# Optimization experiments

Measured on AMD Instinct MI355X. Metric: run time of the kernel, lower is better.

Reference implementation:

```python
import jax, jax.numpy as jnp
import numpy as np

B, D, H, W, C = 2, 8, 56, 56, 384
NH = 12
HD = C // NH
WIN = (2, 7, 7)
SHIFT = (1, 3, 3)
TDIM = 384
RANK = C // 8
HID = 4 * C
N = WIN[0] * WIN[1] * WIN[2]  # 98 tokens per window
NW = (D // WIN[0]) * (H // WIN[1]) * (W // WIN[2])  # windows per batch element


def _rel_index():
    wd, wh, ww = WIN
    coords = np.stack(np.meshgrid(np.arange(wd), np.arange(wh), np.arange(ww), indexing='ij'))
    coords = coords.reshape(3, -1)  # (3, N)
    rel = (coords[:, :, None] - coords[:, None, :]).transpose(1, 2, 0)  # (N, N, 3)
    rel[..., 0] += wd - 1; rel[..., 1] += wh - 1; rel[..., 2] += ww - 1
    rel[..., 0] *= (2 * wh - 1) * (2 * ww - 1)
    rel[..., 1] *= (2 * ww - 1)
    return rel.sum(-1)  # (N, N) int

REL_IDX = _rel_index()


def _wpart_np(x):
    b, d, h, w, c = x.shape
    x = x.reshape(b, d // WIN[0], WIN[0], h // WIN[1], WIN[1], w // WIN[2], WIN[2], c)
    return x.transpose(0, 1, 3, 5, 2, 4, 6, 7).reshape(-1, N, c)


def _attn_mask():
    # faithful port of compute_mask (note: only 2 slices along W, as in source)
    wd, wh, ww = WIN
    sd, sh, sw = SHIFT
    img = np.zeros((1, D, H, W, 1), np.float32)
    cnt = 0
    for ds in (slice(-wd), slice(-wd, -sd), slice(-sd, None)):
        for hs in (slice(-wh), slice(-wh, -sh), slice(-sh, None)):
            for ws in (slice(-ww), slice(-ww, None)):
                img[:, ds, hs, ws, :] = cnt
                cnt += 1
    mw = _wpart_np(img).squeeze(-1)  # (nW, N)
    am = mw[:, None, :] - mw[:, :, None]  # (nW, N, N)
    return np.where(am != 0, np.float32(-100.0), np.float32(0.0))

ATTN_MASK = _attn_mask()


def wpart(x):
    b, c = x.shape[0], x.shape[-1]
    x = x.reshape(b, D // WIN[0], WIN[0], H // WIN[1], WIN[1], W // WIN[2], WIN[2], c)
    return x.transpose(0, 1, 3, 5, 2, 4, 6, 7).reshape(-1, N, c)


def wrev(win):
    c = win.shape[-1]
    x = win.reshape(B, D // WIN[0], H // WIN[1], W // WIN[2], WIN[0], WIN[1], WIN[2], c)
    return x.transpose(0, 1, 4, 2, 5, 3, 6, 7).reshape(B, D, H, W, c)


def ln(x):
    m = x.mean(-1, keepdims=True)
    v = ((x - m) ** 2).mean(-1, keepdims=True)
    return (x - m) / jnp.sqrt(v + 1e-6)


def window_attn(xw, qkv_w, qkv_b, proj_w, proj_b, rel_bias, mask):
    Bw = xw.shape[0]
    qkv = (xw @ qkv_w + qkv_b).reshape(Bw, N, 3, NH, HD).transpose(2, 0, 3, 1, 4)
    q, k, v = qkv[0] * (HD ** -0.5), qkv[1], qkv[2]
    a = jnp.einsum('bhnd,bhmd->bhnm', q, k)  # (Bw, NH, N, N)
    bias = rel_bias[REL_IDX.reshape(-1)].reshape(N, N, NH).transpose(2, 0, 1)
    a = a + bias[None]
    a = a.reshape(Bw // NW, NW, NH, N, N) + mask[None, :, None]
    a = jax.nn.softmax(a.reshape(Bw, NH, N, N), axis=-1)
    out = jnp.einsum('bhnm,bhmd->bhnd', a, v).transpose(0, 2, 1, 3).reshape(Bw, N, C)
    return out @ proj_w + proj_b


def setup_inputs() -> dict:
    key = jax.random.key(0)
    ks = jax.random.split(key, 16)
    s = 0.02
    return {
        'x': jax.random.normal(ks[0], (B, D, H, W, C), jnp.float32),
        't': jax.random.normal(ks[1], (B, TDIM), jnp.float32),
        'qkv_w': jax.random.normal(ks[2], (C, 3 * C), jnp.float32) * s,
        'qkv_b': jax.random.normal(ks[3], (3 * C,), jnp.float32) * s,
        'proj_w': jax.random.normal(ks[4], (C, C), jnp.float32) * s,
        'proj_b': jax.random.normal(ks[5], (C,), jnp.float32) * s,
        'rel_bias': jax.random.normal(ks[6], ((2 * WIN[0] - 1) * (2 * WIN[1] - 1) * (2 * WIN[2] - 1), NH), jnp.float32) * s,
        'fc1_w': jax.random.normal(ks[7], (C, HID), jnp.float32) * s,
        'fc1_b': jax.random.normal(ks[8], (HID,), jnp.float32) * s,
        'fc2_w': jax.random.normal(ks[9], (HID, C), jnp.float32) * s,
        'fc2_b': jax.random.normal(ks[10], (C,), jnp.float32) * s,
        'ada_w1': jax.random.normal(ks[11], (TDIM, RANK), jnp.float32) * s,
        'ada_w2': jax.random.normal(ks[12], (RANK, 6 * C), jnp.float32) * s,
        'ada_b2': jax.random.normal(ks[13], (6 * C,), jnp.float32) * s,
    }


def reference(x, t, qkv_w, qkv_b, proj_w, proj_b, rel_bias, fc1_w, fc1_b, fc2_w, fc2_b, ada_w1, ada_w2, ada_b2):
    mask = jnp.asarray(ATTN_MASK)
    mod = jax.nn.silu(t) @ ada_w1 @ ada_w2 + ada_b2  # (B, 6C)
    s_msa, sc_msa, g_msa, s_mlp, sc_mlp, g_mlp = jnp.split(mod, 6, axis=1)

    def mod5(h, sh, sc):
        return h * (1 + sc[:, None, None, None, :]) + sh[:, None, None, None, :]

    # attention branch (shifted-window MSA)
    h = mod5(ln(x), s_msa, sc_msa)
    hs = jnp.roll(h, shift=(-SHIFT[0], -SHIFT[1], -SHIFT[2]), axis=(1, 2, 3))
    aw = window_attn(wpart(hs), qkv_w, qkv_b, proj_w, proj_b, rel_bias, mask)
    hs = wrev(aw)
    h = jnp.roll(hs, shift=SHIFT, axis=(1, 2, 3))
    x = x + g_msa[:, None, None, None, :] * h

    # MLP branch
    h2 = mod5(ln(x), s_mlp, sc_mlp)
    m = jax.nn.gelu(h2 @ fc1_w + fc1_b, approximate=False) @ fc2_w + fc2_b
    return x + g_mlp[:, None, None, None, :] * m
```

## Files before the change

### kernel.cpp

```cpp
#include <hip/hip_runtime.h>
#include <hip/hip_bf16.h>
#include <math.h>

using bf16 = __hip_bfloat16;
typedef __bf16 bf16x8 __attribute__((ext_vector_type(8)));
typedef float f32x4 __attribute__((ext_vector_type(4)));
typedef unsigned int u32;


__device__ __forceinline__ void async_cp16(const void* g, void* l) {
  __builtin_amdgcn_global_load_lds(
      (const __attribute__((address_space(1))) u32*)g,
      (__attribute__((address_space(3))) u32*)l, 16, 0, 0);
}

__device__ __forceinline__ int row_to_gidx(int row) {
  int win = row / 98, tok = row - win * 98;
  int b = win >> 8, wd = (win >> 6) & 3, wh = (win >> 3) & 7, ww = win & 7;
  int td = tok / 49, rem = tok - td * 49;
  int th = rem / 7, tw = rem - th * 7;
  int od = (wd * 2 + td + 1) & 7;
  int oh = wh * 7 + th + 3; if (oh >= 56) oh -= 56;
  int ow = ww * 7 + tw + 3; if (ow >= 56) ow -= 56;
  return ((b * 8 + od) * 56 + oh) * 56 + ow;
}

__global__ __launch_bounds__(256) void mod_kernel(
    const float* __restrict__ t, const float* __restrict__ w1,
    const float* __restrict__ w2, const float* __restrict__ b2,
    float* __restrict__ modout)
{
  __shared__ float u[2 * 48];
  int tid = threadIdx.x;
  if (tid < 96) {
    int b = tid / 48, r = tid - (tid / 48) * 48;
    float acc = 0.f;
    for (int k = 0; k < 384; ++k) {
      float x = t[b * 384 + k];
      float s = x / (1.f + __expf(-x));
      acc += s * w1[k * 48 + r];
    }
    u[b * 48 + r] = acc;
  }
  __syncthreads();
  for (int idx = tid; idx < 2 * 2304; idx += 256) {
    int b = idx / 2304, c = idx - b * 2304;
    float acc = b2[c];
    #pragma unroll
    for (int k = 0; k < 48; ++k) acc += u[b * 48 + k] * w2[k * 2304 + c];
    modout[idx] = acc;
  }
}

__global__ __launch_bounds__(256) void wconv_frag_kernel(
    const float* __restrict__ W, bf16* __restrict__ Wf, int K, int N)
{
  int idx = blockIdx.x * 256 + threadIdx.x;
  if (idx >= K * N) return;
  int k = idx / N, n = idx - (idx / N) * N;
  int ntile = n >> 4, kstep = k >> 5;
  int l = (n & 15) + (((k >> 3) & 3) << 4);
  size_t dst = (((size_t)(ntile * (K >> 5) + kstep)) << 9) + (l << 3) + (k & 7);
  Wf[dst] = __float2bfloat16(W[idx]);
}

__global__ __launch_bounds__(256) void bm_kernel(
    const float* __restrict__ relb, bf16* __restrict__ bm)
{
  int idx = blockIdx.x * 256 + threadIdx.x;
  if (idx >= 4 * 12 * 112 * 112) return;
  int j = idx % 112, tmp = idx / 112;
  int i = tmp % 112; tmp /= 112;
  int h = tmp % 12, p = tmp / 12;
  float v;
  if (i < 98 && j < 98) {
    int tdi = i / 49, ri = i % 49, thi = ri / 7, twi = ri % 7;
    int tdj = j / 49, rj = j % 49, thj = rj / 7, twj = rj % 7;
    int ridx = (tdi - tdj + 1) * 169 + (thi - thj + 6) * 13 + (twi - twj + 6);
    bool msk = ((p & 2) && (tdi != tdj)) || ((p & 1) && ((thi < 4) != (thj < 4)));
    v = relb[ridx * 12 + h] + (msk ? -100.f : 0.f);
  } else {
    v = -1e38f;
  }
  bm[idx] = __float2bfloat16(v);
}

template <int PHASE>
__global__ __launch_bounds__(256) void ln_mod_kernel(
    const float* __restrict__ src, const float* __restrict__ modv,
    bf16* __restrict__ dst)
{
  int wid = threadIdx.x >> 6, lane = threadIdx.x & 63;
  int row = blockIdx.x * 4 + wid;
  int gtok;
  if (PHASE == 0) gtok = row_to_gidx(row); else gtok = row;
  int b = row / 25088;
  const float* s = src + (size_t)gtok * 384;
  float vals[6], sum = 0.f, sq = 0.f;
  #pragma unroll
  for (int i = 0; i < 6; ++i) {
    float v = s[lane + i * 64];
    vals[i] = v; sum += v; sq += v * v;
  }
  #pragma unroll
  for (int o = 32; o; o >>= 1) { sum += __shfl_xor(sum, o, 64); sq += __shfl_xor(sq, o, 64); }
  float mean = sum * (1.f / 384.f);
  float var = sq * (1.f / 384.f) - mean * mean;
  float rstd = rsqrtf(var + 1e-6f);
  int mb = b * 2304 + (PHASE == 0 ? 0 : 1152);
  #pragma unroll
  for (int i = 0; i < 6; ++i) {
    int c = lane + i * 64;
    float scv = modv[mb + 384 + c], shv = modv[mb + c];
    dst[(size_t)row * 384 + c] = __float2bfloat16((vals[i] - mean) * rstd * (1.f + scv) + shv);
  }
}

template <int EPI>
__global__ __launch_bounds__(256) void gemm128_kernel(
    const bf16* __restrict__ A, const bf16* __restrict__ Bf,
    const float* __restrict__ bias, const int N, const int K,
    bf16* __restrict__ outB, float* __restrict__ outF,
    const float* __restrict__ resid, const float* __restrict__ modv)
{
  __shared__ bf16 sA[2][128 * 32];
  const int tid = threadIdx.x;
  const int lane = tid & 63, wid = tid >> 6;
  const int wm = wid >> 1, wn = wid & 1;

  const int gx = gridDim.x;
  const int nwg = gx * (int)gridDim.y;
  const int orig = (int)blockIdx.y * gx + (int)blockIdx.x;
  const int q = nwg >> 3;
  const int wg = (orig & 7) * q + (orig >> 3);
  const int bx = wg % gx, by = wg / gx;
  const int row0 = by * 128, col0 = bx * 128;

  const int lrow = lane & 15;
  const int sl8 = (((lane >> 4) ^ ((lane >> 1) & 3)) << 3);
  const int r0 = tid >> 2;
  const int c0 = (((tid & 3) ^ ((tid >> 3) & 3)) << 3);

  const int nK32 = K >> 5;
  const bf16* Bfb[4];
  #pragma unroll
  for (int n = 0; n < 4; ++n) {
    const int ntile = (col0 >> 4) + wn * 4 + n;
    Bfb[n] = Bf + (((size_t)(ntile * nK32)) << 9) + (lane << 3);
  }

  const f32x4 vzero = {0.f, 0.f, 0.f, 0.f};
  f32x4 acc[4][4];
  #pragma unroll
  for (int m = 0; m < 4; ++m)
    #pragma unroll
    for (int n = 0; n < 4; ++n) acc[m][n] = vzero;

  const bf16* Arow0 = A + (size_t)(row0 + r0) * K + c0;
  const bf16* Arow1 = A + (size_t)(row0 + r0 + 64) * K + c0;

  auto stage = [&](int b, int kt) {
    async_cp16(Arow0 + kt, &sA[b][(size_t)tid * 8]);
    async_cp16(Arow1 + kt, &sA[b][(size_t)(tid + 256) * 8]);
  };

  stage(0, 0);
  asm volatile("s_waitcnt vmcnt(0)" ::: "memory");
  __syncthreads();
  int cur = 0;
  for (int t = 0; t < nK32; ++t) {
    bf16x8 bfv[4], af[4];
    #pragma unroll
    for (int n = 0; n < 4; ++n)
      bfv[n] = *(const bf16x8*)(Bfb[n] + ((size_t)t << 9));
    if (t + 1 < nK32) stage(cur ^ 1, (t + 1) * 32);
    #pragma unroll
    for (int m = 0; m < 4; ++m)
      af[m] = *(const bf16x8*)(&sA[cur][(wm * 64 + m * 16 + lrow) * 32 + sl8]);
    #pragma unroll
    for (int m = 0; m < 4; ++m)
      #pragma unroll
      for (int n = 0; n < 4; ++n)
        acc[m][n] = __builtin_amdgcn_mfma_f32_16x16x32_bf16(af[m], bfv[n], acc[m][n], 0, 0, 0);
    if (t + 1 < nK32) {
      asm volatile("s_waitcnt vmcnt(0)" ::: "memory");
      __syncthreads();
      cur ^= 1;
    }
  }

  #pragma unroll
  for (int m = 0; m < 4; ++m) {
    #pragma unroll
    for (int r = 0; r < 4; ++r) {
      const int row = row0 + wm * 64 + m * 16 + (lane >> 4) * 4 + r;
      int gofs = 0, b = 0;
      if (EPI == 1) { gofs = row_to_gidx(row) * 384; b = row / 25088; }
      if (EPI == 3) { gofs = row * 384; b = row / 25088; }
      #pragma unroll
      for (int n = 0; n < 4; ++n) {
        const int col = col0 + wn * 64 + n * 16 + (lane & 15);
        float v = acc[m][n][r] + bias[col];
        if (EPI == 0) {
          outB[(size_t)row * N + col] = __float2bfloat16(v);
        } else if (EPI == 2) {
          float g = 0.5f * v * (1.f + erff(v * 0.70710678118654752f));
          outB[(size_t)row * N + col] = __float2bfloat16(g);
        } else if (EPI == 1) {
          outF[gofs + col] = resid[gofs + col] + modv[b * 2304 + 768 + col] * v;
        } else {
          outF[gofs + col] = resid[gofs + col] + modv[b * 2304 + 1920 + col] * v;
        }
      }
    }
  }
}

__global__ __launch_bounds__(256) void attn_kernel(
    const bf16* __restrict__ qkv, const bf16* __restrict__ bm,
    bf16* __restrict__ outp)
{
  __shared__ bf16 k_s[112][40];
  __shared__ bf16 v_t[32][136];
  __shared__ bf16 p_s[4][16][136];

  const int head = blockIdx.x;
  const int win = blockIdx.y;
  const int tid = threadIdx.x;
  const int lane = tid & 63, wid = tid >> 6;
  const int g = lane >> 4, c16 = lane & 15;
  const size_t rowbase = (size_t)win * 98;
  const bf16 zero = __float2bfloat16(0.f);

  for (int lin = tid; lin < 448; lin += 256) {
    int row = lin >> 2, ch = (lin & 3) << 3;
    uint4 val = make_uint4(0, 0, 0, 0);
    if (row < 98)
      val = *(const uint4*)(qkv + (rowbase + row) * 1152 + 384 + head * 32 + ch);
    *(uint4*)&k_s[row][ch] = val;
  }
  for (int lin = tid; lin < 4096; lin += 256) {
    int d = lin & 31, tok = lin >> 5;
    bf16 val = zero;
    if (tok < 98) val = qkv[(rowbase + tok) * 1152 + 768 + head * 32 + d];
    v_t[d][tok] = val;
  }
  for (int lin = tid; lin < 1536; lin += 256) {
    int w = lin / 384, rem = lin - w * 384;
    p_s[w][rem / 24][112 + rem % 24] = zero;
  }
  __syncthreads();

  const int p = ((((win >> 6) & 3) == 3) ? 2 : 0) | ((((win >> 3) & 7) == 7) ? 1 : 0);
  const bf16* bmrow = bm + (size_t)(p * 12 + head) * 12544;
  const float scale = 0.17677669529663687f;
  const f32x4 vzero = {0.f, 0.f, 0.f, 0.f};

  for (int s = wid; s < 7; s += 4) {
    const int q0 = s * 16;
    int qrow = q0 + c16; if (qrow > 97) qrow = 97;
    bf16x8 qf = *(const bf16x8*)(qkv + (rowbase + qrow) * 1152 + head * 32 + g * 8);

    f32x4 sa[7];
    #pragma unroll
    for (int ct = 0; ct < 7; ++ct) {
      bf16x8 kf = *(const bf16x8*)&k_s[ct * 16 + c16][g * 8];
      sa[ct] = __builtin_amdgcn_mfma_f32_16x16x32_bf16(qf, kf, vzero, 0, 0, 0);
    }

    float sv[7][4];
    float mrow[4] = {-1e30f, -1e30f, -1e30f, -1e30f};
    #pragma unroll
    for (int ct = 0; ct < 7; ++ct) {
      #pragma unroll
      for (int r = 0; r < 4; ++r) {
        int i = q0 + g * 4 + r, j = ct * 16 + c16;
        float val = sa[ct][r] * scale + __bfloat162float(bmrow[i * 112 + j]);
        sv[ct][r] = val;
        mrow[r] = fmaxf(mrow[r], val);
      }
    }
    #pragma unroll
    for (int r = 0; r < 4; ++r) {
      #pragma unroll
      for (int off = 1; off < 16; off <<= 1)
        mrow[r] = fmaxf(mrow[r], __shfl_xor(mrow[r], off, 64));
    }
    float rsum[4] = {0.f, 0.f, 0.f, 0.f};
    #pragma unroll
    for (int ct = 0; ct < 7; ++ct) {
      #pragma unroll
      for (int r = 0; r < 4; ++r) {
        float e = __expf(sv[ct][r] - mrow[r]);
        sv[ct][r] = e;
        rsum[r] += e;
      }
    }
    #pragma unroll
    for (int r = 0; r < 4; ++r) {
      #pragma unroll
      for (int off = 1; off < 16; off <<= 1)
        rsum[r] += __shfl_xor(rsum[r], off, 64);
      rsum[r] = 1.f / rsum[r];
    }
    #pragma unroll
    for (int ct = 0; ct < 7; ++ct)
      #pragma unroll
      for (int r = 0; r < 4; ++r)
        p_s[wid][g * 4 + r][ct * 16 + c16] = __float2bfloat16(sv[ct][r] * rsum[r]);

    asm volatile("s_waitcnt lgkmcnt(0)" ::: "memory");

    f32x4 o0 = vzero, o1 = vzero;
    #pragma unroll
    for (int kk = 0; kk < 4; ++kk) {
      bf16x8 pa = *(const bf16x8*)&p_s[wid][c16][kk * 32 + g * 8];
      bf16x8 v0 = *(const bf16x8*)&v_t[c16][kk * 32 + g * 8];
      bf16x8 v1 = *(const bf16x8*)&v_t[16 + c16][kk * 32 + g * 8];
      o0 = __builtin_amdgcn_mfma_f32_16x16x32_bf16(pa, v0, o0, 0, 0, 0);
      o1 = __builtin_amdgcn_mfma_f32_16x16x32_bf16(pa, v1, o1, 0, 0, 0);
    }
    #pragma unroll
    for (int r = 0; r < 4; ++r) {
      int qi = q0 + g * 4 + r;
      if (qi < 98) {
        size_t ob = (rowbase + qi) * 384 + head * 32;
        outp[ob + c16] = __float2bfloat16(o0[r]);
        outp[ob + 16 + c16] = __float2bfloat16(o1[r]);
      }
    }
  }
}

extern "C" void kernel_launch(void* const* d_in, const int* in_sizes, int n_in,
                              void* d_out, int out_size, void* d_ws, size_t ws_size,
                              hipStream_t stream)
{
  (void)in_sizes; (void)n_in; (void)out_size; (void)ws_size;
  const float* x      = (const float*)d_in[0];
  const float* t      = (const float*)d_in[1];
  const float* qkv_w  = (const float*)d_in[2];
  const float* qkv_b  = (const float*)d_in[3];
  const float* proj_w = (const float*)d_in[4];
  const float* proj_b = (const float*)d_in[5];
  const float* relb   = (const float*)d_in[6];
  const float* fc1_w  = (const float*)d_in[7];
  const float* fc1_b  = (const float*)d_in[8];
  const float* fc2_w  = (const float*)d_in[9];
  const float* fc2_b  = (const float*)d_in[10];
  const float* ada_w1 = (const float*)d_in[11];
  const float* ada_w2 = (const float*)d_in[12];
  const float* ada_b2 = (const float*)d_in[13];
  float* out = (float*)d_out;
  char* ws = (char*)d_ws;

  float* modbuf = (float*)(ws + 0);
  bf16* wqkv_t  = (bf16*)(ws + 18432);
  bf16* wproj_t = (bf16*)(ws + 903168);
  bf16* wfc1_t  = (bf16*)(ws + 1198080);
  bf16* wfc2_t  = (bf16*)(ws + 2377728);
  bf16* bufA    = (bf16*)(ws + 3557376);
  bf16* qkvbuf  = (bf16*)(ws + 42092544);
  bf16* bufB    = (bf16*)(ws + 42092544 + 115605504);
  bf16* midbuf  = (bf16*)(ws + 42092544);
  bf16* bmbuf   = bufA;

  wconv_frag_kernel<<<(384 * 1152 + 255) / 256, 256, 0, stream>>>(qkv_w, wqkv_t, 384, 1152);
  wconv_frag_kernel<<<(384 * 384 + 255) / 256, 256, 0, stream>>>(proj_w, wproj_t, 384, 384);
  wconv_frag_kernel<<<(384 * 1536 + 255) / 256, 256, 0, stream>>>(fc1_w, wfc1_t, 384, 1536);
  wconv_frag_kernel<<<(1536 * 384 + 255) / 256, 256, 0, stream>>>(fc2_w, wfc2_t, 1536, 384);

  mod_kernel<<<1, 256, 0, stream>>>(t, ada_w1, ada_w2, ada_b2, modbuf);

  ln_mod_kernel<0><<<12544, 256, 0, stream>>>(x, modbuf, bufA);

  gemm128_kernel<0><<<dim3(9, 392), 256, 0, stream>>>(bufA, wqkv_t, qkv_b, 1152, 384,
                                                      qkvbuf, nullptr, nullptr, nullptr);

  bm_kernel<<<2352, 256, 0, stream>>>(relb, bmbuf);

  attn_kernel<<<dim3(12, 512), 256, 0, stream>>>(qkvbuf, bmbuf, bufB);

  gemm128_kernel<1><<<dim3(3, 392), 256, 0, stream>>>(bufB, wproj_t, proj_b, 384, 384,
                                                      nullptr, out, x, modbuf);

  ln_mod_kernel<1><<<12544, 256, 0, stream>>>(out, modbuf, bufA);

  gemm128_kernel<2><<<dim3(12, 392), 256, 0, stream>>>(bufA, wfc1_t, fc1_b, 1536, 384,
                                                       midbuf, nullptr, nullptr, nullptr);

  gemm128_kernel<3><<<dim3(3, 392), 256, 0, stream>>>(midbuf, wfc2_t, fc2_b, 384, 1536,
                                                      nullptr, out, out, modbuf);
}
```

Baseline: 574.5 us.

## Load GEMM A tiles directly from global into registers with register double-buffering

Replaces the LDS-staged async copies of the A operand in the 128x128 GEMM with direct per-lane global vector loads into registers. Loads for the next K step are double-buffered in registers, which removes the shared memory and the per-iteration barriers. In exchange, each A element is now fetched from global/L2 by both wn waves instead of once per block. The reads are also narrow 16-byte row-strided accesses, and more registers are needed for the two operand buffers.

```diff
diff --git a/kernel.cpp b/kernel.cpp
--- a/kernel.cpp
+++ b/kernel.cpp
@@ -7,12 +7,6 @@
 typedef float f32x4 __attribute__((ext_vector_type(4)));
 typedef unsigned int u32;
 
-
-__device__ __forceinline__ void async_cp16(const void* g, void* l) {
-  __builtin_amdgcn_global_load_lds(
-      (const __attribute__((address_space(1))) u32*)g,
-      (__attribute__((address_space(3))) u32*)l, 16, 0, 0);
-}
 
 __device__ __forceinline__ int row_to_gidx(int row) {
   int win = row / 98, tok = row - win * 98;
@@ -123,7 +117,6 @@
     bf16* __restrict__ outB, float* __restrict__ outF,
     const float* __restrict__ resid, const float* __restrict__ modv)
 {
-  __shared__ bf16 sA[2][128 * 32];
   const int tid = threadIdx.x;
   const int lane = tid & 63, wid = tid >> 6;
   const int wm = wid >> 1, wn = wid & 1;
@@ -136,18 +129,12 @@
   const int bx = wg % gx, by = wg / gx;
   const int row0 = by * 128, col0 = bx * 128;
 
-  const int lrow = lane & 15;
-  const int sl8 = (((lane >> 4) ^ ((lane >> 1) & 3)) << 3);
-  const int r0 = tid >> 2;
-  const int c0 = (((tid & 3) ^ ((tid >> 3) & 3)) << 3);
-
   const int nK32 = K >> 5;
-  const bf16* Bfb[4];
-  #pragma unroll
-  for (int n = 0; n < 4; ++n) {
-    const int ntile = (col0 >> 4) + wn * 4 + n;
-    Bfb[n] = Bf + (((size_t)(ntile * nK32)) << 9) + (lane << 3);
-  }
+
+  const bf16* abase = A + (size_t)(row0 + wm * 64 + (lane & 15)) * K + ((lane >> 4) << 3);
+  const size_t amstride = (size_t)16 * K;
+  const bf16* bbase = Bf + (((size_t)((col0 >> 4) + wn * 4) * nK32) << 9) + (lane << 3);
+  const size_t bnstride = (size_t)nK32 << 9;
 
   const f32x4 vzero = {0.f, 0.f, 0.f, 0.f};
   f32x4 acc[4][4];
@@ -156,38 +143,43 @@
     #pragma unroll
     for (int n = 0; n < 4; ++n) acc[m][n] = vzero;
 
-  const bf16* Arow0 = A + (size_t)(row0 + r0) * K + c0;
-  const bf16* Arow1 = A + (size_t)(row0 + r0 + 64) * K + c0;
-
-  auto stage = [&](int b, int kt) {
-    async_cp16(Arow0 + kt, &sA[b][(size_t)tid * 8]);
-    async_cp16(Arow1 + kt, &sA[b][(size_t)(tid + 256) * 8]);
-  };
-
-  stage(0, 0);
-  asm volatile("s_waitcnt vmcnt(0)" ::: "memory");
-  __syncthreads();
-  int cur = 0;
-  for (int t = 0; t < nK32; ++t) {
-    bf16x8 bfv[4], af[4];
-    #pragma unroll
-    for (int n = 0; n < 4; ++n)
-      bfv[n] = *(const bf16x8*)(Bfb[n] + ((size_t)t << 9));
-    if (t + 1 < nK32) stage(cur ^ 1, (t + 1) * 32);
-    #pragma unroll
-    for (int m = 0; m < 4; ++m)
-      af[m] = *(const bf16x8*)(&sA[cur][(wm * 64 + m * 16 + lrow) * 32 + sl8]);
-    #pragma unroll
-    for (int m = 0; m < 4; ++m)
-      #pragma unroll
-      for (int n = 0; n < 4; ++n)
-        acc[m][n] = __builtin_amdgcn_mfma_f32_16x16x32_bf16(af[m], bfv[n], acc[m][n], 0, 0, 0);
-    if (t + 1 < nK32) {
-      asm volatile("s_waitcnt vmcnt(0)" ::: "memory");
-      __syncthreads();
-      cur ^= 1;
-    }
-  }
+  bf16x8 a0[4], b0[4], a1[4], b1[4];
+
+#define LOAD_A(dst, t)                                                        \
+  {                                                                           \
+    _Pragma("unroll")                                                         \
+    for (int m = 0; m < 4; ++m)                                               \
+      dst[m] = *(const bf16x8*)(abase + m * amstride + (size_t)(t) * 32);     \
+  }
+#define LOAD_B(dst, t)                                                        \
+  {                                                                           \
+    _Pragma("unroll")                                                         \
+    for (int n = 0; n < 4; ++n)                                               \
+      dst[n] = *(const bf16x8*)(bbase + n * bnstride + ((size_t)(t) << 9));   \
+  }
+#define MFMA_STEP(aa, bb)                                                     \
+  {                                                                           \
+    _Pragma("unroll")                                                         \
+    for (int m = 0; m < 4; ++m)                                               \
+      _Pragma("unroll")                                                       \
+      for (int n = 0; n < 4; ++n)                                             \
+        acc[m][n] = __builtin_amdgcn_mfma_f32_16x16x32_bf16(aa[m], bb[n],     \
+                                                            acc[m][n], 0, 0, 0); \
+  }
+
+  LOAD_A(a0, 0); LOAD_B(b0, 0);
+  int t = 0;
+  for (; t + 2 <= nK32; t += 2) {
+    LOAD_A(a1, t + 1); LOAD_B(b1, t + 1);
+    MFMA_STEP(a0, b0);
+    if (t + 2 < nK32) { LOAD_A(a0, t + 2); LOAD_B(b0, t + 2); }
+    MFMA_STEP(a1, b1);
+  }
+  if (t < nK32) { MFMA_STEP(a0, b0); }
+
+#undef LOAD_A
+#undef LOAD_B
+#undef MFMA_STEP
 
   #pragma unroll
   for (int m = 0; m < 4; ++m) {
```

Measured after the change: 730.8 us. +27.2%, slower.
